# Kernel tuning notes

Hardware: AMD Instinct MI355X
Metric: run time of the kernel (lower is better)

The kernel has to match this reference:

```python
import jax, jax.numpy as jnp
import numpy as np

N_U = 100000   # num users
N_V = 50000    # num items
K = 5          # num_support (rating levels)
E_SUP = 400000 # edges per support
E = 500000     # decoder prediction edges
D_IN = 512     # input_dim
D_GCN = 500    # gcn_hidden_dim (D_GCN % K == 0)
D_SIDE = 128   # side_feat_dim
H_SIDE = 64    # side_hidden_dim
D_ENC = 128    # encode_hidden_dim
NB = 3         # num_basis
NC = 5         # num_classes


def setup_inputs() -> dict:
    key = jax.random.key(0)
    ks = jax.random.split(key, 20)
    s = 0.05
    return {
        # sparse supports (COO): user_supports[i] = (N_U,N_V), item_supports[i] = transpose
        "sup_user_idx": jax.random.randint(ks[0], (K, E_SUP), 0, N_U),
        "sup_item_idx": jax.random.randint(ks[1], (K, E_SUP), 0, N_V),
        "sup_vals": jax.random.uniform(ks[2], (K, E_SUP), dtype=jnp.float32),
        "user_inputs": jax.random.normal(ks[3], (N_U, D_IN), dtype=jnp.float32),
        "item_inputs": jax.random.normal(ks[4], (N_V, D_IN), dtype=jnp.float32),
        "user_side_inputs": jax.random.normal(ks[5], (N_U, D_SIDE), dtype=jnp.float32),
        "item_side_inputs": jax.random.normal(ks[6], (N_V, D_SIDE), dtype=jnp.float32),
        "user_edge_idx": jax.random.randint(ks[7], (E,), 0, N_U),
        "item_edge_idx": jax.random.randint(ks[8], (E,), 0, N_V),
        # parameters
        "W_enc": jax.random.normal(ks[9], (K, D_IN, D_GCN // K), dtype=jnp.float32) * s,
        "Wu1": jax.random.normal(ks[10], (D_SIDE, H_SIDE), dtype=jnp.float32) * s,
        "bu1": jnp.zeros((H_SIDE,), dtype=jnp.float32),
        "Wi1": jax.random.normal(ks[11], (D_SIDE, H_SIDE), dtype=jnp.float32) * s,
        "bi1": jnp.zeros((H_SIDE,), dtype=jnp.float32),
        "Wu2": jax.random.normal(ks[12], (D_GCN + H_SIDE, D_ENC), dtype=jnp.float32) * s,
        "Wi2": jax.random.normal(ks[13], (D_GCN + H_SIDE, D_ENC), dtype=jnp.float32) * s,
        "dec_W": jax.random.normal(ks[14], (NB, D_ENC, D_ENC), dtype=jnp.float32) * s,
        "dec_cls": jax.random.normal(ks[15], (NB, NC), dtype=jnp.float32) * s,
    }


def _forward(sup_user_idx, sup_item_idx, sup_vals, user_inputs, item_inputs,
             user_side_inputs, item_side_inputs, user_edge_idx, item_edge_idx,
             W_enc, Wu1, bu1, Wi1, bi1, Wu2, Wi2, dec_W, dec_cls):
    # ---- StackGCNEncoder ----
    tmp_u = jnp.einsum("nd,kdf->knf", user_inputs, W_enc)  # [K, N_U, D_GCN//K]
    tmp_v = jnp.einsum("nd,kdf->knf", item_inputs, W_enc)  # [K, N_V, D_GCN//K]

    def agg_user(rows, cols, vals, xv):  # sparse.mm(user_support, tmp_v)
        return jax.ops.segment_sum(vals[:, None] * xv[cols], rows, num_segments=N_U)

    def agg_item(rows, cols, vals, xu):  # sparse.mm(item_support, tmp_u)
        return jax.ops.segment_sum(vals[:, None] * xu[rows], cols, num_segments=N_V)

    user_hidden = jax.vmap(agg_user)(sup_user_idx, sup_item_idx, sup_vals, tmp_v)  # [K,N_U,f]
    item_hidden = jax.vmap(agg_item)(sup_user_idx, sup_item_idx, sup_vals, tmp_u)  # [K,N_V,f]
    # concat over supports along feature dim
    user_gcn = jax.nn.relu(jnp.transpose(user_hidden, (1, 0, 2)).reshape(N_U, D_GCN))
    item_gcn = jax.nn.relu(jnp.transpose(item_hidden, (1, 0, 2)).reshape(N_V, D_GCN))

    # ---- dense1 (relu, bias) ----
    user_side = jax.nn.relu(user_side_inputs @ Wu1 + bu1)
    item_side = jax.nn.relu(item_side_inputs @ Wi1 + bi1)

    # ---- concat + dense2 (identity activation, no bias) ----
    user_embed = jnp.concatenate([user_gcn, user_side], axis=1) @ Wu2  # [N_U, D_ENC]
    item_embed = jnp.concatenate([item_gcn, item_side], axis=1) @ Wi2  # [N_V, D_ENC]

    # ---- Decoder (bilinear basis, identity activation) ----
    u = user_embed[user_edge_idx]  # [E, D_ENC]
    v = item_embed[item_edge_idx]  # [E, D_ENC]
    basis = jnp.stack([jnp.sum((u @ dec_W[b]) * v, axis=1) for b in range(NB)], axis=1)  # [E, NB]
    return basis @ dec_cls  # [E, NC]


def reference(sup_user_idx, sup_item_idx, sup_vals, user_inputs, item_inputs,
              user_side_inputs, item_side_inputs, user_edge_idx, item_edge_idx,
              W_enc, Wu1, bu1, Wi1, bi1, Wu2, Wi2, dec_W, dec_cls):
    return _forward(sup_user_idx, sup_item_idx, sup_vals, user_inputs, item_inputs,
                    user_side_inputs, item_side_inputs, user_edge_idx, item_edge_idx,
                    W_enc, Wu1, bu1, Wi1, bi1, Wu2, Wi2, dec_W, dec_cls)
```

## Files before the change

kernel.cpp:

```cpp
#include <hip/hip_runtime.h>

#define NU 100000
#define NV 50000
#define KSUP 5
#define ESUP 400000
#define NEDGE (KSUP * ESUP)
#define NE 500000
#define DIN 512
#define DGCN 500
#define FSUP 100
#define DSIDE 128
#define HSIDE 64
#define DENC 128
#define NBAS 3
#define NCLS 5

#define TMPW 640
#define XW 576

#define BNODE 512
#define RU 196
#define RV 98
#define NBU (KSUP * RU)
#define NBV (KSUP * RV)
#define NBT (NBU + NBV)
#define CAPU 2560
#define CAPV 5120
#define CHUNK 8192

#define GU128 782
#define GV128 391
#define GU64 1563
#define GV64 782
#define GBIN 245
#define PB1 (GBIN + 1280)
#define PB2 (PB1 + 288)
#define PB3 (PB2 + 288)
#define PB4 (PB3 + 48)
#define PTOT (PB4 + 75000)

__device__ __forceinline__ ushort f2bf(float x) {
    union { float f; unsigned u; } c; c.f = x;
    unsigned r = (c.u + 0x7FFFu + ((c.u >> 16) & 1u)) >> 16;
    return (ushort)r;
}
__device__ __forceinline__ float lof(uint g) { return __uint_as_float(g << 16); }
__device__ __forceinline__ float hif(uint g) { return __uint_as_float(g & 0xffff0000u); }

typedef __attribute__((ext_vector_type(4))) float f32x4;
typedef __attribute__((ext_vector_type(8))) short bf16x8;
typedef __attribute__((address_space(3))) void lds_void;
typedef const __attribute__((address_space(1))) void glob_void;
typedef unsigned long long ull;

__device__ __forceinline__ void gemm_body(
    const ushort* __restrict__ A, const ushort* __restrict__ BT,
    ushort* __restrict__ Cout, int M, int N, int K, int ldc,
    int rowBase, int colBase)
{
    __shared__ ushort As[128 * 64];
    __shared__ ushort Bs[128 * 64];
    const int t = threadIdx.x;
    const int lane = t & 63;
    const int w = t >> 6;
    const int wr = w >> 1, wc = w & 1;

    f32x4 acc[4][4] = {};

    for (int k0 = 0; k0 < K; k0 += 64) {
        #pragma unroll
        for (int i = 0; i < 4; ++i) {
            int chi = i * 256 + t;
            int r = chi >> 3;
            int c = (((chi >> 3) & 7) ^ (chi & 7)) * 8;
            int ga = rowBase + r; if (ga > M - 1) ga = M - 1;
            __builtin_amdgcn_global_load_lds(
                (glob_void*)(A + (size_t)ga * K + k0 + c),
                (lds_void*)(As + (size_t)chi * 8), 16, 0, 0);
            int gb = colBase + r; if (gb > N - 1) gb = N - 1;
            __builtin_amdgcn_global_load_lds(
                (glob_void*)(BT + (size_t)gb * K + k0 + c),
                (lds_void*)(Bs + (size_t)chi * 8), 16, 0, 0);
        }
        __syncthreads();

        #pragma unroll
        for (int kk = 0; kk < 2; ++kk) {
            bf16x8 af[4], bfr[4];
            const int cb2 = (kk * 32 + (lane >> 4) * 8) * 2;
            #pragma unroll
            for (int mi = 0; mi < 4; ++mi) {
                int r = wr * 64 + mi * 16 + (lane & 15);
                int off = (r * 128 + cb2) ^ ((r & 7) << 4);
                af[mi] = *(const bf16x8*)((const char*)As + off);
            }
            #pragma unroll
            for (int nj = 0; nj < 4; ++nj) {
                int r = wc * 64 + nj * 16 + (lane & 15);
                int off = (r * 128 + cb2) ^ ((r & 7) << 4);
                bfr[nj] = *(const bf16x8*)((const char*)Bs + off);
            }
            #pragma unroll
            for (int mi = 0; mi < 4; ++mi)
                #pragma unroll
                for (int nj = 0; nj < 4; ++nj)
                    acc[mi][nj] = __builtin_amdgcn_mfma_f32_16x16x32_bf16(
                        af[mi], bfr[nj], acc[mi][nj], 0, 0, 0);
        }
        __syncthreads();
    }

    #pragma unroll
    for (int mi = 0; mi < 4; ++mi) {
        #pragma unroll
        for (int q = 0; q < 4; ++q) {
            int gr = rowBase + wr * 64 + mi * 16 + (lane >> 4) * 4 + q;
            if (gr >= M) continue;
            #pragma unroll
            for (int nj = 0; nj < 4; ++nj) {
                int gc = colBase + wc * 64 + nj * 16 + (lane & 15);
                Cout[(size_t)gr * ldc + gc] = f2bf(acc[mi][nj][q]);
            }
        }
    }
}

__global__ __launch_bounds__(256) void gemm_bf16_k(
    const ushort* __restrict__ A, const ushort* __restrict__ BT,
    ushort* __restrict__ Cout, int M, int N, int K, int ldc)
{
    gemm_body(A, BT, Cout, M, N, K, ldc, blockIdx.y * 128, blockIdx.x * 128);
}

__global__ __launch_bounds__(256) void gemm_enc_k(
    const ushort* __restrict__ u_bf, const ushort* __restrict__ v_bf,
    const ushort* __restrict__ WencT2,
    ushort* __restrict__ tmpU, ushort* __restrict__ tmpV)
{
    int y = blockIdx.y;
    const ushort* A; ushort* C; int M, rowBase;
    if (y < GU128) { A = u_bf; C = tmpU; M = NU; rowBase = y * 128; }
    else           { A = v_bf; C = tmpV; M = NV; rowBase = (y - GU128) * 128; }
    gemm_body(A, WencT2, C, M, TMPW, 512, TMPW, rowBase, blockIdx.x * 128);
}

__global__ __launch_bounds__(256) void gemm_d2_k(
    const ushort* __restrict__ Xu, const ushort* __restrict__ Xv,
    const ushort* __restrict__ W2u, const ushort* __restrict__ W2i,
    ushort* __restrict__ embU, ushort* __restrict__ embV)
{
    int y = blockIdx.y;
    const ushort* A; const ushort* BT; ushort* C; int M, rowBase;
    if (y < GU128) { A = Xu; BT = W2u; C = embU; M = NU; rowBase = y * 128; }
    else           { A = Xv; BT = W2i; C = embV; M = NV; rowBase = (y - GU128) * 128; }
    gemm_body(A, BT, C, M, DENC, XW, DENC, rowBase, 0);
}

#define BM 64
#define BN 64
#define BK 16
__device__ __forceinline__ void side_body(
    const float* __restrict__ A, const float* __restrict__ B,
    const float* __restrict__ bias, ushort* __restrict__ X,
    int M, int K, int rowBase)
{
    __shared__ float As[BK][BM + 4];
    __shared__ float Bs[BK][BN + 4];
    const int t = threadIdx.x;
    const int ty = t >> 4, tx = t & 15;
    float acc[4][4] = {};

    for (int k0 = 0; k0 < K; k0 += BK) {
        #pragma unroll
        for (int p = 0; p < 4; ++p) {
            int r = p * 16 + (t >> 4), kk = t & 15;
            int gr = rowBase + r, gk = k0 + kk;
            As[kk][r] = (gr < M && gk < K) ? A[(size_t)gr * K + gk] : 0.f;
        }
        #pragma unroll
        for (int p = 0; p < 4; ++p) {
            int kk = p * 4 + (t >> 6), j = t & 63;
            int gk = k0 + kk;
            Bs[kk][j] = (j < HSIDE && gk < K) ? B[(size_t)gk * HSIDE + j] : 0.f;
        }
        __syncthreads();
        #pragma unroll
        for (int kk = 0; kk < BK; ++kk) {
            float4 a4 = *reinterpret_cast<const float4*>(&As[kk][ty * 4]);
            float4 b4 = *reinterpret_cast<const float4*>(&Bs[kk][tx * 4]);
            float aa[4] = {a4.x, a4.y, a4.z, a4.w};
            float bb[4] = {b4.x, b4.y, b4.z, b4.w};
            #pragma unroll
            for (int i = 0; i < 4; ++i)
                #pragma unroll
                for (int j = 0; j < 4; ++j)
                    acc[i][j] = fmaf(aa[i], bb[j], acc[i][j]);
        }
        __syncthreads();
    }
    #pragma unroll
    for (int i = 0; i < 4; ++i) {
        int gr = rowBase + ty * 4 + i;
        if (gr >= M) continue;
        #pragma unroll
        for (int j = 0; j < 4; ++j) {
            int gc = tx * 4 + j;
            if (gc < HSIDE)
                X[(size_t)gr * XW + 500 + gc] = f2bf(fmaxf(acc[i][j] + bias[gc], 0.f));
        }
    }
}

__global__ __launch_bounds__(256) void side_k(
    const float* __restrict__ uS, const float* __restrict__ vS,
    const float* __restrict__ Wu1, const float* __restrict__ bu1,
    const float* __restrict__ Wi1, const float* __restrict__ bi1,
    ushort* __restrict__ Xu, ushort* __restrict__ Xv)
{
    int b = blockIdx.x;
    const float *A, *B, *bias; ushort* X; int M, rowBase;
    if (b < GU64) { A = uS; B = Wu1; bias = bu1; X = Xu; M = NU; rowBase = b * 64; }
    else          { A = vS; B = Wi1; bias = bi1; X = Xv; M = NV; rowBase = (b - GU64) * 64; }
    side_body(A, B, bias, X, M, DSIDE, rowBase);
}

__global__ __launch_bounds__(256) void prep_k(
    const int* __restrict__ su, const int* __restrict__ si,
    const float* __restrict__ sv,
    int* __restrict__ bCnt, ull* __restrict__ bktU, ull* __restrict__ bktV,
    const float* __restrict__ W_enc, ushort* __restrict__ WencT2,
    const float* __restrict__ Wu2, const float* __restrict__ Wi2,
    ushort* __restrict__ W2ufT, ushort* __restrict__ W2ifT,
    const float* __restrict__ dec_W, ushort* __restrict__ decbf,
    const float* __restrict__ u_in, const float* __restrict__ v_in,
    ushort* __restrict__ u_bf, ushort* __restrict__ v_bf)
{
    __shared__ int lcnt[NBT];
    __shared__ int lbase[NBT];
    const int bid = blockIdx.x;
    const int t = threadIdx.x;

    if (bid < GBIN) {
        const int e0 = bid * CHUNK;
        for (int i = t; i < NBT; i += 256) lcnt[i] = 0;
        __syncthreads();
        for (int i = t; i < CHUNK; i += 256) {
            int e = e0 + i;
            if (e >= NEDGE) break;
            int k = e / ESUP;
            int r = su[e], c = si[e];
            atomicAdd(&lcnt[k * RU + (r >> 9)], 1);
            atomicAdd(&lcnt[NBU + k * RV + (c >> 9)], 1);
        }
        __syncthreads();
        for (int i = t; i < NBT; i += 256) {
            int n = lcnt[i];
            lbase[i] = n ? atomicAdd(&bCnt[i], n) : 0;
        }
        __syncthreads();
        for (int i = t; i < NBT; i += 256) lcnt[i] = 0;
        __syncthreads();
        for (int i = t; i < CHUNK; i += 256) {
            int e = e0 + i;
            if (e >= NEDGE) break;
            int k = e / ESUP;
            int r = su[e], c = si[e];
            ull vb = (ull)(unsigned)__float_as_int(sv[e]) << 32;
            int bu = k * RU + (r >> 9);
            int pu = lbase[bu] + atomicAdd(&lcnt[bu], 1);
            if (pu < CAPU)
                bktU[(size_t)bu * CAPU + pu] = vb | (uint)(((r & 511) << 16) | c);
            int bv = NBU + k * RV + (c >> 9);
            int pv = lbase[bv] + atomicAdd(&lcnt[bv], 1);
            if (pv < CAPV)
                bktV[(size_t)(bv - NBU) * CAPV + pv] = vb | (uint)(((c & 511) << 17) | r);
        }
    } else if (bid < PB1) {
        int idx = (bid - GBIN) * 256 + t;
        int np = idx >> 9, d = idx & 511;
        int k = np >> 7, f = np & 127;
        float v = (f < FSUP) ? W_enc[((size_t)k * DIN + d) * FSUP + f] : 0.f;
        WencT2[idx] = f2bf(v);
    } else if (bid < PB3) {
        int which = (bid < PB2) ? 0 : 1;
        int idx = (bid - (which ? PB2 : PB1)) * 256 + t;
        const float* W = which ? Wi2 : Wu2;
        ushort* out = which ? W2ifT : W2ufT;
        int j = idx / XW, c = idx - j * XW;
        float v = (c < DGCN + HSIDE) ? W[(size_t)c * DENC + j] : 0.f;
        out[idx] = f2bf(v);
    } else if (bid < PB4) {
        long i = ((long)(bid - PB3) * 256 + t) * 4;
        if (i < (long)NBAS * DENC * DENC) {
            float4 v = *(const float4*)(dec_W + i);
            ushort4 o;
            o.x = f2bf(v.x); o.y = f2bf(v.y); o.z = f2bf(v.z); o.w = f2bf(v.w);
            *(ushort4*)(decbf + i) = o;
        }
    } else {
        long i = ((long)(bid - PB4) * 256 + t) * 4;
        const long nu = (long)NU * 512;
        const float* src; ushort* dst;
        if (i < nu) { src = u_in; dst = u_bf; }
        else {
            i -= nu;
            if (i >= (long)NV * 512) return;
            src = v_in; dst = v_bf;
        }
        float4 v = *(const float4*)(src + i);
        ushort4 o;
        o.x = f2bf(v.x); o.y = f2bf(v.y); o.z = f2bf(v.z); o.w = f2bf(v.w);
        *(ushort4*)(dst + i) = o;
    }
}

__global__ __launch_bounds__(256) void bscan_k(const int* __restrict__ bCnt,
                                               int* __restrict__ bBase,
                                               int* __restrict__ rowPtrU,
                                               int* __restrict__ rowPtrV) {
    __shared__ int sm[256];
    const int t = threadIdx.x;
    const int PER = (NBT + 255) / 256;
    int loc[6]; int s = 0;
    #pragma unroll
    for (int i = 0; i < PER; ++i) {
        int idx = t * PER + i;
        loc[i] = (idx < NBT) ? bCnt[idx] : 0;
        s += loc[i];
    }
    sm[t] = s; __syncthreads();
    int sv = s;
    for (int off = 1; off < 256; off <<= 1) {
        int add = (t >= off) ? sm[t - off] : 0;
        __syncthreads();
        sm[t] += add;
        __syncthreads();
    }
    int base = sm[t] - sv;
    int run = 0;
    #pragma unroll
    for (int i = 0; i < PER; ++i) {
        int idx = t * PER + i;
        if (idx < NBT) bBase[idx] = base + run;
        run += loc[i];
    }
    if (t == 0) {
        rowPtrU[KSUP * NU] = NEDGE;
        rowPtrV[KSUP * NV] = NEDGE;
    }
}

__global__ __launch_bounds__(256) void scat3_k(
    const int* __restrict__ bCnt, const int* __restrict__ bBase,
    const ull* __restrict__ bktU, const ull* __restrict__ bktV,
    int* __restrict__ rowPtrU, int* __restrict__ rowPtrV,
    ull* __restrict__ eU, ull* __restrict__ eV)
{
    __shared__ ull stage[CAPV];
    __shared__ int cnt[BNODE];
    __shared__ int rowOff[BNODE];
    __shared__ int part[256];
    const int t = threadIdx.x;
    const int b = blockIdx.x;
    const int isU = (b < NBU);
    const ull* src;
    int n, k, baseN, base, NN;
    int* rp;
    if (isU) {
        k = b / RU; baseN = (b % RU) << 9;
        src = bktU + (size_t)b * CAPU;
        n = bCnt[b]; if (n > CAPU) n = CAPU;
        base = bBase[b]; NN = NU; rp = rowPtrU;
    } else {
        int bb = b - NBU;
        k = bb / RV; baseN = (bb % RV) << 9;
        src = bktV + (size_t)bb * CAPV;
        n = bCnt[b]; if (n > CAPV) n = CAPV;
        base = bBase[b] - NEDGE; NN = NV; rp = rowPtrV;
    }

    for (int i = t; i < BNODE; i += 256) cnt[i] = 0;
    __syncthreads();

    for (int i = t; i < n; i += 256) {
        ull en = __builtin_nontemporal_load(&src[i]);
        uint w0 = (uint)en;
        int local = isU ? (int)(w0 >> 16) : (int)(w0 >> 17);
        atomicAdd(&cnt[local], 1);
    }
    __syncthreads();

    int c0 = cnt[2 * t], c1 = cnt[2 * t + 1];
    int s = c0 + c1;
    part[t] = s;
    __syncthreads();
    for (int off = 1; off < 256; off <<= 1) {
        int add = (t >= off) ? part[t - off] : 0;
        __syncthreads();
        part[t] += add;
        __syncthreads();
    }
    int excl = part[t] - s;
    cnt[2 * t] = excl;          rowOff[2 * t] = excl;
    cnt[2 * t + 1] = excl + c0; rowOff[2 * t + 1] = excl + c0;
    __syncthreads();

    for (int i = t; i < BNODE; i += 256) {
        int node = baseN + i;
        if (node < NN) rp[k * NN + node] = base + rowOff[i];
    }

    for (int i = t; i < n; i += 256) {
        ull en = __builtin_nontemporal_load(&src[i]);
        uint w0 = (uint)en;
        int local; uint off4;
        if (isU) { local = (int)(w0 >> 16); off4 = (w0 & 0xFFFF) * (TMPW * 2); }
        else     { local = (int)(w0 >> 17); off4 = (w0 & 0x1FFFF) * (TMPW * 2); }
        int p = atomicAdd(&cnt[local], 1);
        stage[p] = (en & 0xFFFFFFFF00000000ull) | off4;
    }
    __syncthreads();

    ull* dst = (isU ? eU : eV) + base;
    for (int i = t; i < n; i += 256)
        __builtin_nontemporal_store(stage[i], &dst[i]);
}

template<int K0, int NK, int B, int NNODE>
__device__ __forceinline__ void agg_do(
    const int* __restrict__ rowPtr, const ull* __restrict__ eArr,
    const char* __restrict__ tSrc, int n, uint lane4,
    float* __restrict__ a0, float* __restrict__ a1)
{
    int s[NK], d[NK];
    #pragma unroll
    for (int kk = 0; kk < NK; ++kk) {
        int g = (K0 + kk) * NNODE + n;
        int ss = rowPtr[g];
        int ee = rowPtr[g + 1];
        s[kk] = ss; d[kk] = ee - ss;
    }
    uint ex[NK][B], ev[NK][B], gw[NK][B];
    #pragma unroll
    for (int kk = 0; kk < NK; ++kk)
        #pragma unroll
        for (int i = 0; i < B; ++i) {
            int idx = (i < d[kk]) ? i : 0;
            ull t = __builtin_nontemporal_load(&eArr[s[kk] + idx]);
            ex[kk][i] = (i < d[kk]) ? (uint)t : 0u;
            ev[kk][i] = (uint)(t >> 32);
        }
    #pragma unroll
    for (int kk = 0; kk < NK; ++kk)
        #pragma unroll
        for (int i = 0; i < B; ++i)
            gw[kk][i] = *(const uint*)(tSrc + (ex[kk][i] + lane4 + ((uint)(K0 + kk) << 8)));
    #pragma unroll
    for (int kk = 0; kk < NK; ++kk) {
        float x0 = 0.f, x1 = 0.f;
        #pragma unroll
        for (int i = 0; i < B; ++i)
            if (i < d[kk]) {
                float v = __uint_as_float(ev[kk][i]);
                x0 = fmaf(v, lof(gw[kk][i]), x0);
                x1 = fmaf(v, hif(gw[kk][i]), x1);
            }
        a0[K0 + kk] = x0; a1[K0 + kk] = x1;
    }
    #pragma unroll
    for (int kk = 0; kk < NK; ++kk) {
        if (d[kk] > B) {
            uint fx[B], fv[B], g1[B];
            #pragma unroll
            for (int i = 0; i < B; ++i) {
                int idx = (B + i < d[kk]) ? B + i : B;
                ull t = __builtin_nontemporal_load(&eArr[s[kk] + idx]);
                fx[i] = (B + i < d[kk]) ? (uint)t : 0u;
                fv[i] = (uint)(t >> 32);
            }
            #pragma unroll
            for (int i = 0; i < B; ++i)
                g1[i] = *(const uint*)(tSrc + (fx[i] + lane4 + ((uint)(K0 + kk) << 8)));
            #pragma unroll
            for (int i = 0; i < B; ++i)
                if (B + i < d[kk]) {
                    float v = __uint_as_float(fv[i]);
                    a0[K0 + kk] = fmaf(v, lof(g1[i]), a0[K0 + kk]);
                    a1[K0 + kk] = fmaf(v, hif(g1[i]), a1[K0 + kk]);
                }
            for (int p = 2 * B; p < d[kk]; ++p) {
                ull t = __builtin_nontemporal_load(&eArr[s[kk] + p]);
                uint g = *(const uint*)(tSrc + ((uint)t + lane4 + ((uint)(K0 + kk) << 8)));
                float v = __uint_as_float((uint)(t >> 32));
                a0[K0 + kk] = fmaf(v, lof(g), a0[K0 + kk]);
                a1[K0 + kk] = fmaf(v, hif(g), a1[K0 + kk]);
            }
        }
    }
}

__device__ __forceinline__ void agg_store(ushort* Xrow, int lane,
                                          const float* a0, const float* a1) {
    #pragma unroll
    for (int k = 0; k < KSUP; ++k) {
        uint payload = (uint)f2bf(fmaxf(a0[k], 0.f)) |
                       ((uint)f2bf(fmaxf(a1[k], 0.f)) << 16);
        if (lane < 50)
            __builtin_nontemporal_store(payload, (uint*)(Xrow + k * FSUP) + lane);
    }
    if (lane < 6)
        __builtin_nontemporal_store(0u, (uint*)(Xrow + 564) + lane);
}

__global__ __launch_bounds__(256) void agg_u_k(
    const int* __restrict__ rowPtrU, const ull* __restrict__ eU,
    const ushort* __restrict__ tmpV, ushort* __restrict__ Xu)
{
    const int lane = threadIdx.x & 63;
    const int n = blockIdx.x * 4 + (threadIdx.x >> 6);
    const uint lane4 = (uint)(((lane < 50) ? lane : 49) << 2);
    float a0[KSUP], a1[KSUP];
    agg_do<0, KSUP, 4, NU>(rowPtrU, eU, (const char*)tmpV, n, lane4, a0, a1);
    agg_store(Xu + (size_t)n * XW, lane, a0, a1);
}

__global__ __launch_bounds__(256) void agg_v_k(
    const int* __restrict__ rowPtrV, const ull* __restrict__ eV,
    const ushort* __restrict__ tmpU, ushort* __restrict__ Xv)
{
    const int lane = threadIdx.x & 63;
    const int n = blockIdx.x * 4 + (threadIdx.x >> 6);
    const uint lane4 = (uint)(((lane < 50) ? lane : 49) << 2);
    float a0[KSUP], a1[KSUP];
    agg_do<0, 3, 8, NV>(rowPtrV, eV, (const char*)tmpU, n, lane4, a0, a1);
    agg_do<3, 2, 8, NV>(rowPtrV, eV, (const char*)tmpU, n, lane4, a0, a1);
    agg_store(Xv + (size_t)n * XW, lane, a0, a1);
}

__global__ __launch_bounds__(256) void dec_k(
    const int* __restrict__ ue, const int* __restrict__ ie,
    const ushort* __restrict__ embU, const ushort* __restrict__ Vb,
    const float* __restrict__ cls, float* __restrict__ out, int nE)
{
    int e = blockIdx.x * 8 + (threadIdx.x >> 5);
    if (e >= nE) return;
    int lane = threadIdx.x & 31;
    int u = ue[e], v = ie[e];
    const int2* pu2 = (const int2*)(embU + (size_t)u * DENC);
    const int2* pv2 = (const int2*)(Vb + (size_t)v * (NBAS * DENC));
    int2 uu = pu2[lane];
    int2 bb[NBAS];
    #pragma unroll
    for (int b = 0; b < NBAS; ++b) bb[b] = pv2[b * 32 + lane];
    float uxl = lof((uint)uu.x), uxh = hif((uint)uu.x);
    float uyl = lof((uint)uu.y), uyh = hif((uint)uu.y);
    float s[NBAS];
    #pragma unroll
    for (int b = 0; b < NBAS; ++b) {
        float t = lof((uint)bb[b].x) * uxl;
        t = fmaf(hif((uint)bb[b].x), uxh, t);
        t = fmaf(lof((uint)bb[b].y), uyl, t);
        s[b] = fmaf(hif((uint)bb[b].y), uyh, t);
    }
    #pragma unroll
    for (int off = 16; off; off >>= 1)
        #pragma unroll
        for (int b = 0; b < NBAS; ++b) s[b] += __shfl_xor(s[b], off, 32);
    if (lane < NCLS) {
        float o = 0.f;
        #pragma unroll
        for (int b = 0; b < NBAS; ++b) o += s[b] * cls[b * NCLS + lane];
        out[(size_t)e * NCLS + lane] = o;
    }
}

extern "C" void kernel_launch(void* const* d_in, const int* in_sizes, int n_in,
                              void* d_out, int out_size, void* d_ws, size_t ws_size,
                              hipStream_t stream) {
    const int*   sup_u  = (const int*)  d_in[0];
    const int*   sup_i  = (const int*)  d_in[1];
    const float* sup_v  = (const float*)d_in[2];
    const float* u_in   = (const float*)d_in[3];
    const float* v_in   = (const float*)d_in[4];
    const float* u_side = (const float*)d_in[5];
    const float* v_side = (const float*)d_in[6];
    const int*   ue     = (const int*)  d_in[7];
    const int*   ie     = (const int*)  d_in[8];
    const float* W_enc  = (const float*)d_in[9];
    const float* Wu1    = (const float*)d_in[10];
    const float* bu1    = (const float*)d_in[11];
    const float* Wi1    = (const float*)d_in[12];
    const float* bi1    = (const float*)d_in[13];
    const float* Wu2    = (const float*)d_in[14];
    const float* Wi2    = (const float*)d_in[15];
    const float* dec_W  = (const float*)d_in[16];
    const float* deccls = (const float*)d_in[17];

    char* ws = (char*)d_ws;
    ushort* u_bf   = (ushort*)(ws);
    ushort* v_bf   = (ushort*)(ws + 102400000LL);
    ushort* Xu     = (ushort*)(ws);
    ushort* Xv     = (ushort*)(ws + 115200000LL);
    int*    rowPtrU= (int*)(ws + 179000000LL);
    int*    rowPtrV= (int*)(ws + 181200000LL);
    int*    bBase  = (int*)(ws + 185780000LL);
    int*    bCnt   = (int*)(ws + 185810000LL);
    ull*    eU     = (ull*)(ws + 186000000LL);
    ull*    eV     = (ull*)(ws + 202000000LL);
    ushort* tmpU   = (ushort*)(ws + 220000000LL);
    ushort* tmpV   = (ushort*)(ws + 348000000LL);
    ull*    bktU   = (ull*)(ws + 220000000LL);
    ull*    bktV   = (ull*)(ws + 241000000LL);
    ushort* embUbf = (ushort*)(ws + 176000000LL);
    ushort* embVbf = (ushort*)(ws + 202000000LL);
    ushort* Vb     = (ushort*)(ws + 220000000LL);
    ushort* WencT2 = (ushort*)(ws + 412000000LL);
    ushort* W2ufT  = (ushort*)(ws + 413000000LL);
    ushort* W2ifT  = (ushort*)(ws + 413200000LL);
    ushort* decbf  = (ushort*)(ws + 413400000LL);

    dim3 blk(256);

    hipMemsetAsync(bCnt, 0, 8192, stream);
    prep_k<<<dim3(PTOT), blk, 0, stream>>>(
        sup_u, sup_i, sup_v, bCnt, bktU, bktV,
        W_enc, WencT2, Wu2, Wi2, W2ufT, W2ifT, dec_W, decbf,
        u_in, v_in, u_bf, v_bf);
    bscan_k<<<dim3(1), blk, 0, stream>>>(bCnt, bBase, rowPtrU, rowPtrV);
    scat3_k<<<dim3(NBT), blk, 0, stream>>>(bCnt, bBase, bktU, bktV,
                                           rowPtrU, rowPtrV, eU, eV);

    gemm_enc_k<<<dim3(TMPW / 128, GU128 + GV128), blk, 0, stream>>>(
        u_bf, v_bf, WencT2, tmpU, tmpV);

    agg_u_k<<<dim3(NU / 4), blk, 0, stream>>>(rowPtrU, eU, tmpV, Xu);
    agg_v_k<<<dim3(NV / 4), blk, 0, stream>>>(rowPtrV, eV, tmpU, Xv);

    side_k<<<dim3(GU64 + GV64), blk, 0, stream>>>(
        u_side, v_side, Wu1, bu1, Wi1, bi1, Xu, Xv);

    gemm_d2_k<<<dim3(1, GU128 + GV128), blk, 0, stream>>>(
        Xu, Xv, W2ufT, W2ifT, embUbf, embVbf);

    gemm_bf16_k<<<dim3(3, GV128), blk, 0, stream>>>(embVbf, decbf, Vb, NV, 384, 128, 384);

    dec_k<<<dim3(NE / 8), blk, 0, stream>>>(ue, ie, embUbf, Vb, deccls, (float*)d_out, NE);
}
```

Measured before the change: 869.9 us.

## Fuse fp32-to-bf16 input conversion into encoder GEMM and merge small kernels

The encoder GEMM now reads fp32 user/item inputs directly and converts them to bf16 while staging into LDS, removing a separate conversion pass that wrote a full bf16 copy of the inputs. The single-block bucket scan kernel is folded into each scatter block, which recomputes the prefix sum redundantly, and the side dense layer is appended as extra blocks of the aggregation kernels. These changes cut kernel launches and a large memory round trip. The cost is register-based loads for A in place of direct global-to-LDS loads, the GEMM re-reading fp32 A once per column tile, and redundant scan work in every scatter block.

```diff
diff --git a/kernel.cpp b/kernel.cpp
--- a/kernel.cpp
+++ b/kernel.cpp
@@ -37,7 +37,6 @@
 #define PB2 (PB1 + 288)
 #define PB3 (PB2 + 288)
 #define PB4 (PB3 + 48)
-#define PTOT (PB4 + 75000)
 
 __device__ __forceinline__ ushort f2bf(float x) {
     union { float f; unsigned u; } c; c.f = x;
@@ -53,8 +52,9 @@
 typedef const __attribute__((address_space(1))) void glob_void;
 typedef unsigned long long ull;
 
+template<int AF32>
 __device__ __forceinline__ void gemm_body(
-    const ushort* __restrict__ A, const ushort* __restrict__ BT,
+    const void* __restrict__ Aptr, const ushort* __restrict__ BT,
     ushort* __restrict__ Cout, int M, int N, int K, int ldc,
     int rowBase, int colBase)
 {
@@ -72,15 +72,30 @@
         for (int i = 0; i < 4; ++i) {
             int chi = i * 256 + t;
             int r = chi >> 3;
-            int c = (((chi >> 3) & 7) ^ (chi & 7)) * 8;
-            int ga = rowBase + r; if (ga > M - 1) ga = M - 1;
-            __builtin_amdgcn_global_load_lds(
-                (glob_void*)(A + (size_t)ga * K + k0 + c),
-                (lds_void*)(As + (size_t)chi * 8), 16, 0, 0);
+            int j = chi & 7;
+            int c = (j ^ (r & 7)) * 8;
             int gb = colBase + r; if (gb > N - 1) gb = N - 1;
             __builtin_amdgcn_global_load_lds(
                 (glob_void*)(BT + (size_t)gb * K + k0 + c),
                 (lds_void*)(Bs + (size_t)chi * 8), 16, 0, 0);
+            int ga = rowBase + r; if (ga > M - 1) ga = M - 1;
+            if constexpr (AF32) {
+                const float* A = (const float*)Aptr;
+                const float* src = A + (size_t)ga * K + k0 + c;
+                float4 a0 = *(const float4*)src;
+                float4 a1 = *(const float4*)(src + 4);
+                bf16x8 pk;
+                pk[0] = (short)f2bf(a0.x); pk[1] = (short)f2bf(a0.y);
+                pk[2] = (short)f2bf(a0.z); pk[3] = (short)f2bf(a0.w);
+                pk[4] = (short)f2bf(a1.x); pk[5] = (short)f2bf(a1.y);
+                pk[6] = (short)f2bf(a1.z); pk[7] = (short)f2bf(a1.w);
+                *(bf16x8*)(As + (size_t)chi * 8) = pk;
+            } else {
+                const ushort* A = (const ushort*)Aptr;
+                __builtin_amdgcn_global_load_lds(
+                    (glob_void*)(A + (size_t)ga * K + k0 + c),
+                    (lds_void*)(As + (size_t)chi * 8), 16, 0, 0);
+            }
         }
         __syncthreads();
 
@@ -129,19 +144,19 @@
     const ushort* __restrict__ A, const ushort* __restrict__ BT,
     ushort* __restrict__ Cout, int M, int N, int K, int ldc)
 {
-    gemm_body(A, BT, Cout, M, N, K, ldc, blockIdx.y * 128, blockIdx.x * 128);
+    gemm_body<0>(A, BT, Cout, M, N, K, ldc, blockIdx.y * 128, blockIdx.x * 128);
 }
 
 __global__ __launch_bounds__(256) void gemm_enc_k(
-    const ushort* __restrict__ u_bf, const ushort* __restrict__ v_bf,
+    const float* __restrict__ u_in, const float* __restrict__ v_in,
     const ushort* __restrict__ WencT2,
     ushort* __restrict__ tmpU, ushort* __restrict__ tmpV)
 {
     int y = blockIdx.y;
-    const ushort* A; ushort* C; int M, rowBase;
-    if (y < GU128) { A = u_bf; C = tmpU; M = NU; rowBase = y * 128; }
-    else           { A = v_bf; C = tmpV; M = NV; rowBase = (y - GU128) * 128; }
-    gemm_body(A, WencT2, C, M, TMPW, 512, TMPW, rowBase, blockIdx.x * 128);
+    const float* A; ushort* C; int M, rowBase;
+    if (y < GU128) { A = u_in; C = tmpU; M = NU; rowBase = y * 128; }
+    else           { A = v_in; C = tmpV; M = NV; rowBase = (y - GU128) * 128; }
+    gemm_body<1>(A, WencT2, C, M, TMPW, 512, TMPW, rowBase, blockIdx.x * 128);
 }
 
 __global__ __launch_bounds__(256) void gemm_d2_k(
@@ -153,11 +168,10 @@
     const ushort* A; const ushort* BT; ushort* C; int M, rowBase;
     if (y < GU128) { A = Xu; BT = W2u; C = embU; M = NU; rowBase = y * 128; }
     else           { A = Xv; BT = W2i; C = embV; M = NV; rowBase = (y - GU128) * 128; }
-    gemm_body(A, BT, C, M, DENC, XW, DENC, rowBase, 0);
+    gemm_body<0>(A, BT, C, M, DENC, XW, DENC, rowBase, 0);
 }
 
 #define BM 64
-#define BN 64
 #define BK 16
 __device__ __forceinline__ void side_body(
     const float* __restrict__ A, const float* __restrict__ B,
@@ -165,7 +179,7 @@
     int M, int K, int rowBase)
 {
     __shared__ float As[BK][BM + 4];
-    __shared__ float Bs[BK][BN + 4];
+    __shared__ float Bs[BK][BM + 4];
     const int t = threadIdx.x;
     const int ty = t >> 4, tx = t & 15;
     float acc[4][4] = {};
@@ -209,19 +223,6 @@
                 X[(size_t)gr * XW + 500 + gc] = f2bf(fmaxf(acc[i][j] + bias[gc], 0.f));
         }
     }
-}
-
-__global__ __launch_bounds__(256) void side_k(
-    const float* __restrict__ uS, const float* __restrict__ vS,
-    const float* __restrict__ Wu1, const float* __restrict__ bu1,
-    const float* __restrict__ Wi1, const float* __restrict__ bi1,
-    ushort* __restrict__ Xu, ushort* __restrict__ Xv)
-{
-    int b = blockIdx.x;
-    const float *A, *B, *bias; ushort* X; int M, rowBase;
-    if (b < GU64) { A = uS; B = Wu1; bias = bu1; X = Xu; M = NU; rowBase = b * 64; }
-    else          { A = vS; B = Wi1; bias = bi1; X = Xv; M = NV; rowBase = (b - GU64) * 64; }
-    side_body(A, B, bias, X, M, DSIDE, rowBase);
 }
 
 __global__ __launch_bounds__(256) void prep_k(
@@ -231,9 +232,7 @@
     const float* __restrict__ W_enc, ushort* __restrict__ WencT2,
     const float* __restrict__ Wu2, const float* __restrict__ Wi2,
     ushort* __restrict__ W2ufT, ushort* __restrict__ W2ifT,
-    const float* __restrict__ dec_W, ushort* __restrict__ decbf,
-    const float* __restrict__ u_in, const float* __restrict__ v_in,
-    ushort* __restrict__ u_bf, ushort* __restrict__ v_bf)
+    const float* __restrict__ dec_W, ushort* __restrict__ decbf)
 {
     __shared__ int lcnt[NBT];
     __shared__ int lbase[NBT];
@@ -289,7 +288,7 @@
         int j = idx / XW, c = idx - j * XW;
         float v = (c < DGCN + HSIDE) ? W[(size_t)c * DENC + j] : 0.f;
         out[idx] = f2bf(v);
-    } else if (bid < PB4) {
+    } else {
         long i = ((long)(bid - PB3) * 256 + t) * 4;
         if (i < (long)NBAS * DENC * DENC) {
             float4 v = *(const float4*)(dec_W + i);
@@ -297,61 +296,11 @@
             o.x = f2bf(v.x); o.y = f2bf(v.y); o.z = f2bf(v.z); o.w = f2bf(v.w);
             *(ushort4*)(decbf + i) = o;
         }
-    } else {
-        long i = ((long)(bid - PB4) * 256 + t) * 4;
-        const long nu = (long)NU * 512;
-        const float* src; ushort* dst;
-        if (i < nu) { src = u_in; dst = u_bf; }
-        else {
-            i -= nu;
-            if (i >= (long)NV * 512) return;
-            src = v_in; dst = v_bf;
-        }
-        float4 v = *(const float4*)(src + i);
-        ushort4 o;
-        o.x = f2bf(v.x); o.y = f2bf(v.y); o.z = f2bf(v.z); o.w = f2bf(v.w);
-        *(ushort4*)(dst + i) = o;
-    }
-}
-
-__global__ __launch_bounds__(256) void bscan_k(const int* __restrict__ bCnt,
-                                               int* __restrict__ bBase,
-                                               int* __restrict__ rowPtrU,
-                                               int* __restrict__ rowPtrV) {
-    __shared__ int sm[256];
-    const int t = threadIdx.x;
-    const int PER = (NBT + 255) / 256;
-    int loc[6]; int s = 0;
-    #pragma unroll
-    for (int i = 0; i < PER; ++i) {
-        int idx = t * PER + i;
-        loc[i] = (idx < NBT) ? bCnt[idx] : 0;
-        s += loc[i];
-    }
-    sm[t] = s; __syncthreads();
-    int sv = s;
-    for (int off = 1; off < 256; off <<= 1) {
-        int add = (t >= off) ? sm[t - off] : 0;
-        __syncthreads();
-        sm[t] += add;
-        __syncthreads();
-    }
-    int base = sm[t] - sv;
-    int run = 0;
-    #pragma unroll
-    for (int i = 0; i < PER; ++i) {
-        int idx = t * PER + i;
-        if (idx < NBT) bBase[idx] = base + run;
-        run += loc[i];
-    }
-    if (t == 0) {
-        rowPtrU[KSUP * NU] = NEDGE;
-        rowPtrV[KSUP * NV] = NEDGE;
     }
 }
 
 __global__ __launch_bounds__(256) void scat3_k(
-    const int* __restrict__ bCnt, const int* __restrict__ bBase,
+    const int* __restrict__ bCnt,
     const ull* __restrict__ bktU, const ull* __restrict__ bktV,
     int* __restrict__ rowPtrU, int* __restrict__ rowPtrV,
     ull* __restrict__ eU, ull* __restrict__ eV)
@@ -360,9 +309,42 @@
     __shared__ int cnt[BNODE];
     __shared__ int rowOff[BNODE];
     __shared__ int part[256];
+    __shared__ int bbl[NBT];
     const int t = threadIdx.x;
     const int b = blockIdx.x;
     const int isU = (b < NBU);
+
+    {
+        const int PER = (NBT + 255) / 256;
+        int loc[6]; int ssum = 0;
+        #pragma unroll
+        for (int i = 0; i < PER; ++i) {
+            int idx = t * PER + i;
+            loc[i] = (idx < NBT) ? bCnt[idx] : 0;
+            ssum += loc[i];
+        }
+        part[t] = ssum; __syncthreads();
+        for (int off = 1; off < 256; off <<= 1) {
+            int add = (t >= off) ? part[t - off] : 0;
+            __syncthreads();
+            part[t] += add;
+            __syncthreads();
+        }
+        int bb = part[t] - ssum;
+        int run = 0;
+        #pragma unroll
+        for (int i = 0; i < PER; ++i) {
+            int idx = t * PER + i;
+            if (idx < NBT) bbl[idx] = bb + run;
+            run += loc[i];
+        }
+        __syncthreads();
+    }
+    if (b == 0 && t == 0) {
+        rowPtrU[KSUP * NU] = NEDGE;
+        rowPtrV[KSUP * NV] = NEDGE;
+    }
+
     const ull* src;
     int n, k, baseN, base, NN;
     int* rp;
@@ -370,13 +352,13 @@
         k = b / RU; baseN = (b % RU) << 9;
         src = bktU + (size_t)b * CAPU;
         n = bCnt[b]; if (n > CAPU) n = CAPU;
-        base = bBase[b]; NN = NU; rp = rowPtrU;
+        base = bbl[b]; NN = NU; rp = rowPtrU;
     } else {
-        int bb = b - NBU;
-        k = bb / RV; baseN = (bb % RV) << 9;
-        src = bktV + (size_t)bb * CAPV;
+        int bb2 = b - NBU;
+        k = bb2 / RV; baseN = (bb2 % RV) << 9;
+        src = bktV + (size_t)bb2 * CAPV;
         n = bCnt[b]; if (n > CAPV) n = CAPV;
-        base = bBase[b] - NEDGE; NN = NV; rp = rowPtrV;
+        base = bbl[b] - NEDGE; NN = NV; rp = rowPtrV;
     }
 
     for (int i = t; i < BNODE; i += 256) cnt[i] = 0;
@@ -514,27 +496,41 @@
 
 __global__ __launch_bounds__(256) void agg_u_k(
     const int* __restrict__ rowPtrU, const ull* __restrict__ eU,
-    const ushort* __restrict__ tmpV, ushort* __restrict__ Xu)
-{
-    const int lane = threadIdx.x & 63;
-    const int n = blockIdx.x * 4 + (threadIdx.x >> 6);
-    const uint lane4 = (uint)(((lane < 50) ? lane : 49) << 2);
-    float a0[KSUP], a1[KSUP];
-    agg_do<0, KSUP, 4, NU>(rowPtrU, eU, (const char*)tmpV, n, lane4, a0, a1);
-    agg_store(Xu + (size_t)n * XW, lane, a0, a1);
+    const ushort* __restrict__ tmpV, ushort* __restrict__ Xu,
+    const float* __restrict__ u_side, const float* __restrict__ Wu1,
+    const float* __restrict__ bu1)
+{
+    int b = blockIdx.x;
+    if (b < NU / 4) {
+        const int lane = threadIdx.x & 63;
+        const int n = b * 4 + (threadIdx.x >> 6);
+        const uint lane4 = (uint)(((lane < 50) ? lane : 49) << 2);
+        float a0[KSUP], a1[KSUP];
+        agg_do<0, KSUP, 4, NU>(rowPtrU, eU, (const char*)tmpV, n, lane4, a0, a1);
+        agg_store(Xu + (size_t)n * XW, lane, a0, a1);
+    } else {
+        side_body(u_side, Wu1, bu1, Xu, NU, DSIDE, (b - NU / 4) * 64);
+    }
 }
 
 __global__ __launch_bounds__(256) void agg_v_k(
     const int* __restrict__ rowPtrV, const ull* __restrict__ eV,
-    const ushort* __restrict__ tmpU, ushort* __restrict__ Xv)
-{
-    const int lane = threadIdx.x & 63;
-    const int n = blockIdx.x * 4 + (threadIdx.x >> 6);
-    const uint lane4 = (uint)(((lane < 50) ? lane : 49) << 2);
-    float a0[KSUP], a1[KSUP];
-    agg_do<0, 3, 8, NV>(rowPtrV, eV, (const char*)tmpU, n, lane4, a0, a1);
-    agg_do<3, 2, 8, NV>(rowPtrV, eV, (const char*)tmpU, n, lane4, a0, a1);
-    agg_store(Xv + (size_t)n * XW, lane, a0, a1);
+    const ushort* __restrict__ tmpU, ushort* __restrict__ Xv,
+    const float* __restrict__ v_side, const float* __restrict__ Wi1,
+    const float* __restrict__ bi1)
+{
+    int b = blockIdx.x;
+    if (b < NV / 4) {
+        const int lane = threadIdx.x & 63;
+        const int n = b * 4 + (threadIdx.x >> 6);
+        const uint lane4 = (uint)(((lane < 50) ? lane : 49) << 2);
+        float a0[KSUP], a1[KSUP];
+        agg_do<0, 3, 8, NV>(rowPtrV, eV, (const char*)tmpU, n, lane4, a0, a1);
+        agg_do<3, 2, 8, NV>(rowPtrV, eV, (const char*)tmpU, n, lane4, a0, a1);
+        agg_store(Xv + (size_t)n * XW, lane, a0, a1);
+    } else {
+        side_body(v_side, Wi1, bi1, Xv, NV, DSIDE, (b - NV / 4) * 64);
+    }
 }
 
 __global__ __launch_bounds__(256) void dec_k(
@@ -597,13 +593,10 @@
     const float* deccls = (const float*)d_in[17];
 
     char* ws = (char*)d_ws;
-    ushort* u_bf   = (ushort*)(ws);
-    ushort* v_bf   = (ushort*)(ws + 102400000LL);
     ushort* Xu     = (ushort*)(ws);
     ushort* Xv     = (ushort*)(ws + 115200000LL);
     int*    rowPtrU= (int*)(ws + 179000000LL);
     int*    rowPtrV= (int*)(ws + 181200000LL);
-    int*    bBase  = (int*)(ws + 185780000LL);
     int*    bCnt   = (int*)(ws + 185810000LL);
     ull*    eU     = (ull*)(ws + 186000000LL);
     ull*    eV     = (ull*)(ws + 202000000LL);
@@ -622,22 +615,19 @@
     dim3 blk(256);
 
     hipMemsetAsync(bCnt, 0, 8192, stream);
-    prep_k<<<dim3(PTOT), blk, 0, stream>>>(
+    prep_k<<<dim3(PB4), blk, 0, stream>>>(
         sup_u, sup_i, sup_v, bCnt, bktU, bktV,
-        W_enc, WencT2, Wu2, Wi2, W2ufT, W2ifT, dec_W, decbf,
-        u_in, v_in, u_bf, v_bf);
-    bscan_k<<<dim3(1), blk, 0, stream>>>(bCnt, bBase, rowPtrU, rowPtrV);
-    scat3_k<<<dim3(NBT), blk, 0, stream>>>(bCnt, bBase, bktU, bktV,
+        W_enc, WencT2, Wu2, Wi2, W2ufT, W2ifT, dec_W, decbf);
+    scat3_k<<<dim3(NBT), blk, 0, stream>>>(bCnt, bktU, bktV,
                                            rowPtrU, rowPtrV, eU, eV);
 
     gemm_enc_k<<<dim3(TMPW / 128, GU128 + GV128), blk, 0, stream>>>(
-        u_bf, v_bf, WencT2, tmpU, tmpV);
-
-    agg_u_k<<<dim3(NU / 4), blk, 0, stream>>>(rowPtrU, eU, tmpV, Xu);
-    agg_v_k<<<dim3(NV / 4), blk, 0, stream>>>(rowPtrV, eV, tmpU, Xv);
-
-    side_k<<<dim3(GU64 + GV64), blk, 0, stream>>>(
-        u_side, v_side, Wu1, bu1, Wi1, bi1, Xu, Xv);
+        u_in, v_in, WencT2, tmpU, tmpV);
+
+    agg_u_k<<<dim3(NU / 4 + GU64), blk, 0, stream>>>(
+        rowPtrU, eU, tmpV, Xu, u_side, Wu1, bu1);
+    agg_v_k<<<dim3(NV / 4 + GV64), blk, 0, stream>>>(
+        rowPtrV, eV, tmpU, Xv, v_side, Wi1, bi1);
 
     gemm_d2_k<<<dim3(1, GU128 + GV128), blk, 0, stream>>>(
         Xu, Xv, W2ufT, W2ifT, embUbf, embVbf);
```

Result: slower. 941.9 us (+8.3%).
